# Kernel tuning notes

Measured on AMD Instinct MI355X. Metric: run time of the kernel, lower is better.

The kernel has to match this reference:

```python
import jax, jax.numpy as jnp
import numpy as np

ROWS, COLS, BATCH, NC, DEG = 256, 512, 512, 5, 16
N = (ROWS + COLS) * BATCH            # total nodes
E = ROWS * DEG * BATCH               # total edges
EPS = 1e-07

def _idx_sets():
    blk = np.arange(BATCH)[:, None] * (ROWS + COLS)
    idx_check = (blk + np.arange(ROWS)[None, :]).ravel()          # index_one
    idx_var = (blk + ROWS + np.arange(COLS)[None, :]).ravel()      # index_two
    return jnp.asarray(idx_check, jnp.int32), jnp.asarray(idx_var, jnp.int32)

IDX_CHECK, IDX_VAR = _idx_sets()

def setup_inputs() -> dict:
    key = jax.random.key(0)
    ks = jax.random.split(key, 18)
    rng = np.random.default_rng(0)
    # per-graph block offsets; row0 = check node ids, row1 = variable ids BEFORE the +ROWS shift
    offs = np.repeat(np.arange(BATCH) * (ROWS + COLS), ROWS * DEG)
    src = offs + rng.integers(0, ROWS, size=E)
    dst = offs + rng.integers(0, COLS, size=E)
    edge_index = jnp.asarray(np.stack([src, dst]), jnp.int32)
    x = jax.random.normal(ks[0], (N, 1), jnp.float32)

    def p(k, shape, fan):
        return (jax.random.uniform(k, shape, jnp.float32) * 2.0 - 1.0) / np.sqrt(fan)

    inp = {"x": x, "edge_index": edge_index}
    for li, base in ((1, 1), (2, 9)):
        inp[f"w1_{li}"] = p(ks[base + 0], (10, 2), 2)
        inp[f"b1_{li}"] = p(ks[base + 1], (10,), 2)
        inp[f"w2_{li}"] = p(ks[base + 2], (1, 10), 10)
        inp[f"b2_{li}"] = p(ks[base + 3], (1,), 10)
        inp[f"wih_{li}"] = p(ks[base + 4], (3, 1), 1)
        inp[f"whh_{li}"] = p(ks[base + 5], (3, 1), 1)
        inp[f"bih_{li}"] = p(ks[base + 6], (3,), 1)
        inp[f"bhh_{li}"] = p(ks[base + 7], (3,), 1)
    return inp

def _ggc(h, j_idx, i_idx, agg_idx, upd_idx, w1, b1, w2, b2, wih, whh, bih, bhh):
    # message: mlp(cat[x_j, x_i])
    feat = jnp.concatenate([h[j_idx], h[i_idx]], axis=1)          # [E,2]
    hid = jax.nn.relu(feat @ w1.T + b1)                            # [E,10]
    msg = hid @ w2.T + b2                                          # [E,1]
    m = jax.ops.segment_sum(msg, agg_idx, num_segments=N)          # scatter-add -> [N,1]
    # GRUCell(input=h[idx], hx=m[idx])   (note: original passes old state as INPUT, message as HIDDEN)
    xg = h[upd_idx]
    hx = m[upd_idx]
    gi = xg @ wih.T + bih                                          # [K,3]
    gh = hx @ whh.T + bhh                                          # [K,3]
    r = jax.nn.sigmoid(gi[:, 0:1] + gh[:, 0:1])
    z = jax.nn.sigmoid(gi[:, 1:2] + gh[:, 1:2])
    n = jnp.tanh(gi[:, 2:3] + r * gh[:, 2:3])
    hnew = (1.0 - z) * n + z * hx
    return h.at[upd_idx].set(hnew)

def reference(x, edge_index, w1_1, b1_1, w2_1, b2_1, wih_1, whh_1, bih_1, bhh_1,
              w1_2, b1_2, w2_2, b2_2, wih_2, whh_2, bih_2, bhh_2):
    src = edge_index[0]
    dst = edge_index[1] + ROWS          # shift variable ids into node index space
    h = x
    for _ in range(NC):
        # ggc1: source_to_target -> x_j=h[src], x_i=h[dst], aggregate at dst, update variable nodes
        h = _ggc(h, src, dst, dst, IDX_VAR, w1_1, b1_1, w2_1, b2_1, wih_1, whh_1, bih_1, bhh_1)
        # ggc2: target_to_source -> x_j=h[dst], x_i=h[src], aggregate at src, update check nodes
        h = _ggc(h, dst, src, src, IDX_CHECK, w1_2, b1_2, w2_2, b2_2, wih_2, whh_2, bih_2, bhh_2)
    return jnp.clip(jax.nn.sigmoid(-h), EPS, 1.0 - EPS)
```

## Files before the change

kernel.cpp:

```cpp
#include <hip/hip_runtime.h>

#define ROWS 256
#define COLS 512
#define BATCH 512
#define NC 5
#define DEG 16
#define EPG (ROWS * DEG)
#define NPG (ROWS + COLS)
#define NT 512
#define EPT (EPG / NT)
#define EPSF 1e-7f
#define MV_W (EPG + 3 * COLS)
#define MC_W (EPG + 3 * ROWS)

typedef unsigned short u16;
typedef unsigned int   u32;
typedef float v2f __attribute__((ext_vector_type(2)));

__device__ __forceinline__ float sigmoid_f(float a) {
    return 1.0f / (1.0f + __expf(-a));
}
__device__ __forceinline__ float tanh_f(float a) {
    return fmaf(2.0f, 1.0f / (1.0f + __expf(-2.0f * a)), -1.0f);
}

__global__ __launch_bounds__(NT, 4) void gnni_kernel(
    const float* __restrict__ x,
    const int*   __restrict__ eidx,
    const float* __restrict__ w1_1, const float* __restrict__ b1_1,
    const float* __restrict__ w2_1, const float* __restrict__ b2_1,
    const float* __restrict__ wih_1, const float* __restrict__ whh_1,
    const float* __restrict__ bih_1, const float* __restrict__ bhh_1,
    const float* __restrict__ w1_2, const float* __restrict__ b1_2,
    const float* __restrict__ w2_2, const float* __restrict__ b2_2,
    const float* __restrict__ wih_2, const float* __restrict__ whh_2,
    const float* __restrict__ bih_2, const float* __restrict__ bhh_2,
    float* __restrict__ out)
{
    __shared__ float msgV[MV_W];
    __shared__ float msgC[MC_W];
    __shared__ u32  cntd[COLS];
    __shared__ u32  cnts[ROWS];
    __shared__ u16  beg_v[COLS];
    __shared__ u16  deg_v[COLS];
    __shared__ u16  beg_c[ROWS];
    __shared__ u16  deg_c[ROWS];
    __shared__ float hc[ROWS];
    __shared__ float hv[COLS];
    __shared__ u32  wsum[8];
    __shared__ u32  wsum2[4];

    const int tid  = threadIdx.x;
    const int lane = tid & 63;
    const int wid  = tid >> 6;
    const int b    = blockIdx.x;
    const int base = b * NPG;
    const long ebase = (long)b * EPG;

    const int4 sa = *(const int4*)(eidx + ebase + tid * 8);
    const int4 sb = *(const int4*)(eidx + ebase + tid * 8 + 4);
    const int4 da = *(const int4*)(eidx + (long)BATCH * EPG + ebase + tid * 8);
    const int4 db = *(const int4*)(eidx + (long)BATCH * EPG + ebase + tid * 8 + 4);
    const int sarr[EPT] = {sa.x, sa.y, sa.z, sa.w, sb.x, sb.y, sb.z, sb.w};
    const int darr[EPT] = {da.x, da.y, da.z, da.w, db.x, db.y, db.z, db.w};
    u32 ep[EPT];
    #pragma unroll
    for (int i = 0; i < EPT; ++i)
        ep[i] = (u32)(sarr[i] - base) | ((u32)(darr[i] - base) << 16);

    for (int i = tid; i < MV_W; i += NT) msgV[i] = 0.0f;
    for (int i = tid; i < MC_W; i += NT) msgC[i] = 0.0f;
    cntd[tid] = 0;
    if (tid < ROWS) cnts[tid] = 0;
    __syncthreads();

    #pragma unroll
    for (int i = 0; i < EPT; ++i) {
        atomicAdd(&cntd[ep[i] >> 16], 1u);
        atomicAdd(&cnts[ep[i] & 0xffffu], 1u);
    }
    __syncthreads();

    u32 myd = cntd[tid];
    u32 acd = (myd + 3u) & ~3u;
    u32 scv = acd;
    #pragma unroll
    for (int st = 1; st < 64; st <<= 1) {
        u32 t = __shfl_up(scv, st);
        if (lane >= st) scv += t;
    }
    if (lane == 63) wsum[wid] = scv;
    u32 mys = 0, acs = 0, scc = 0;
    if (tid < ROWS) {
        mys = cnts[tid];
        acs = (mys + 3u) & ~3u;
        scc = acs;
        #pragma unroll
        for (int st = 1; st < 64; st <<= 1) {
            u32 t = __shfl_up(scc, st);
            if (lane >= st) scc += t;
        }
        if (lane == 63) wsum2[wid] = scc;
    }
    __syncthreads();
    if (tid < 8) {
        u32 v = wsum[tid];
        #pragma unroll
        for (int st = 1; st < 8; st <<= 1) {
            u32 t = __shfl_up(v, st);
            if (tid >= st) v += t;
        }
        wsum[tid] = v;
    } else if (tid < 12) {
        u32 v = wsum2[tid - 8];
        #pragma unroll
        for (int st = 1; st < 4; st <<= 1) {
            u32 t = __shfl_up(v, st);
            if (tid - 8 >= st) v += t;
        }
        wsum2[tid - 8] = v;
    }
    __syncthreads();
    {
        u32 inc  = scv + (wid ? wsum[wid - 1] : 0u);
        u32 begv = inc - acd;
        beg_v[tid] = (u16)begv;
        deg_v[tid] = (u16)myd;
        cntd[tid]  = begv;
    }
    if (tid < ROWS) {
        u32 inc  = scc + (wid ? wsum2[wid - 1] : 0u);
        u32 begc = inc - acs;
        beg_c[tid] = (u16)begc;
        deg_c[tid] = (u16)mys;
        cnts[tid]  = begc;
        hc[tid] = x[base + tid];
    }
    float hvreg = x[base + ROWS + tid];
    hv[tid] = hvreg;
    __syncthreads();

    u32 aS[EPT], aD[EPT], p1B[EPT], p2B[EPT];
    #pragma unroll
    for (int i = 0; i < EPT; ++i) {
        const u32 p = ep[i];
        const u32 s = p & 0xffffu;
        const u32 d = p >> 16;
        aS[i]  = s << 2;
        aD[i]  = d << 2;
        p1B[i] = atomicAdd(&cntd[d], 1u) << 2;
        p2B[i] = atomicAdd(&cnts[s], 1u) << 2;
    }

    v2f A1[5], C1[5], B1[5], W1[5], A2[5], C2[5], B2[5], W2[5];
    #pragma unroll
    for (int j = 0; j < 5; ++j) {
        A1[j] = (v2f){w1_1[4*j],     w1_1[4*j + 2]};
        C1[j] = (v2f){w1_1[4*j + 1], w1_1[4*j + 3]};
        B1[j] = (v2f){b1_1[2*j],     b1_1[2*j + 1]};
        W1[j] = (v2f){w2_1[2*j],     w2_1[2*j + 1]};
        A2[j] = (v2f){w1_2[4*j],     w1_2[4*j + 2]};
        C2[j] = (v2f){w1_2[4*j + 1], w1_2[4*j + 3]};
        B2[j] = (v2f){b1_2[2*j],     b1_2[2*j + 1]};
        W2[j] = (v2f){w2_2[2*j],     w2_2[2*j + 1]};
    }
    const float b2_1s = b2_1[0], b2_2s = b2_2[0];
    const v2f zero2 = (v2f){0.0f, 0.0f};
    const char* const hcB   = (const char*)hc;
    const char* const hvB   = (const char*)hv;
    char*       const msgVB = (char*)msgV;
    char*       const msgCB = (char*)msgC;

    for (int it = 0; it < NC; ++it) {
        float hcs[EPT];
        #pragma unroll
        for (int i = 0; i < EPT; ++i) hcs[i] = *(const float*)(hcB + aS[i]);

        #pragma unroll
        for (int i = 0; i < EPT; ++i) {
            const float xj = hcs[i];
            const float xi = *(const float*)(hvB + aD[i]);
            const v2f xj2 = (v2f){xj, xj}, xi2 = (v2f){xi, xi};
            v2f acc = (v2f){b2_1s, 0.0f};
            #pragma unroll
            for (int j = 0; j < 5; ++j) {
                v2f t = __builtin_elementwise_fma(C1[j], xi2, B1[j]);
                t = __builtin_elementwise_fma(A1[j], xj2, t);
                t = __builtin_elementwise_max(t, zero2);
                acc = __builtin_elementwise_fma(W1[j], t, acc);
            }
            *(float*)(msgVB + p1B[i]) = acc.x + acc.y;
        }
        __syncthreads();

        {
            const int beg = beg_v[tid];
            const int deg = deg_v[tid];
            const float4* mp = (const float4*)&msgV[beg];
            float4 a4 = {0.0f, 0.0f, 0.0f, 0.0f};
            #pragma unroll
            for (int k = 0; k < 5; ++k) {
                if (4 * k < deg) {
                    const float4 q = mp[k];
                    a4.x += q.x; a4.y += q.y; a4.z += q.z; a4.w += q.w;
                }
            }
            float hx = (a4.x + a4.y) + (a4.z + a4.w);
            for (int e = beg + 20; e < beg + deg; ++e) hx += msgV[e];
            const float xg = hvreg;
            float gi0 = fmaf(wih_1[0], xg, bih_1[0]);
            float gi1 = fmaf(wih_1[1], xg, bih_1[1]);
            float gi2 = fmaf(wih_1[2], xg, bih_1[2]);
            float gh0 = fmaf(whh_1[0], hx, bhh_1[0]);
            float gh1 = fmaf(whh_1[1], hx, bhh_1[1]);
            float gh2 = fmaf(whh_1[2], hx, bhh_1[2]);
            float r = sigmoid_f(gi0 + gh0);
            float z = sigmoid_f(gi1 + gh1);
            float n = tanh_f(fmaf(r, gh2, gi2));
            hvreg = fmaf(1.0f - z, n, z * hx);
            hv[tid] = hvreg;
        }
        __syncthreads();

        #pragma unroll
        for (int i = 0; i < EPT; ++i) {
            const float xi = hcs[i];
            const float xj = *(const float*)(hvB + aD[i]);
            const v2f xj2 = (v2f){xj, xj}, xi2 = (v2f){xi, xi};
            v2f acc = (v2f){b2_2s, 0.0f};
            #pragma unroll
            for (int j = 0; j < 5; ++j) {
                v2f t = __builtin_elementwise_fma(C2[j], xi2, B2[j]);
                t = __builtin_elementwise_fma(A2[j], xj2, t);
                t = __builtin_elementwise_max(t, zero2);
                acc = __builtin_elementwise_fma(W2[j], t, acc);
            }
            *(float*)(msgCB + p2B[i]) = acc.x + acc.y;
        }
        __syncthreads();

        {
            const int c    = tid >> 1;
            const int half = tid & 1;
            const int beg = beg_c[c];
            const int deg = deg_c[c];
            const float4* mp = (const float4*)&msgC[beg];
            float4 a4 = {0.0f, 0.0f, 0.0f, 0.0f};
            #pragma unroll
            for (int k = 0; k < 4; ++k) {
                const int ch = half + 2 * k;
                if (4 * ch < deg) {
                    const float4 q = mp[ch];
                    a4.x += q.x; a4.y += q.y; a4.z += q.z; a4.w += q.w;
                }
            }
            float part = (a4.x + a4.y) + (a4.z + a4.w);
            for (int e = beg + 32 + half; e < beg + deg; e += 2) part += msgC[e];
            part += __shfl_xor(part, 1);
            if (half == 0) {
                const float hx = part;
                const float xg = hc[c];
                float gi0 = fmaf(wih_2[0], xg, bih_2[0]);
                float gi1 = fmaf(wih_2[1], xg, bih_2[1]);
                float gi2 = fmaf(wih_2[2], xg, bih_2[2]);
                float gh0 = fmaf(whh_2[0], hx, bhh_2[0]);
                float gh1 = fmaf(whh_2[1], hx, bhh_2[1]);
                float gh2 = fmaf(whh_2[2], hx, bhh_2[2]);
                float r = sigmoid_f(gi0 + gh0);
                float z = sigmoid_f(gi1 + gh1);
                float n = tanh_f(fmaf(r, gh2, gi2));
                hc[c] = fmaf(1.0f - z, n, z * hx);
            }
        }
        __syncthreads();
    }

    {
        float sgm = 1.0f / (1.0f + __expf(hvreg));
        out[base + ROWS + tid] = fminf(fmaxf(sgm, EPSF), 1.0f - EPSF);
    }
    if (tid < ROWS) {
        float sgm = 1.0f / (1.0f + __expf(hc[tid]));
        out[base + tid] = fminf(fmaxf(sgm, EPSF), 1.0f - EPSF);
    }
}

extern "C" void kernel_launch(void* const* d_in, const int* in_sizes, int n_in,
                              void* d_out, int out_size, void* d_ws, size_t ws_size,
                              hipStream_t stream) {
    const float* x    = (const float*)d_in[0];
    const int*   eidx = (const int*)d_in[1];
    gnni_kernel<<<BATCH, NT, 0, stream>>>(
        x, eidx,
        (const float*)d_in[2],  (const float*)d_in[3],
        (const float*)d_in[4],  (const float*)d_in[5],
        (const float*)d_in[6],  (const float*)d_in[7],
        (const float*)d_in[8],  (const float*)d_in[9],
        (const float*)d_in[10], (const float*)d_in[11],
        (const float*)d_in[12], (const float*)d_in[13],
        (const float*)d_in[14], (const float*)d_in[15],
        (const float*)d_in[16], (const float*)d_in[17],
        (float*)d_out);
}
```

Measured before the change: 38.44 us.

## Double threads per block and split edge and reduction work across more lanes

Raises the block size from 512 to 1024 threads, so each thread handles 4 edges instead of 8. The variable-node reduction is now split across 2 lanes and the check-node reduction across 4 lanes, combined with shuffles. The count-scan phases are remapped onto separate wave ranges, and the final output write is unified. The aim is to shorten the serial per-iteration work within each graph block by using more waves per CU. The cost is more lanes idling in the GRU update phases and higher register and occupancy pressure at 1024 threads with the unchanged launch bounds.

```diff
diff --git a/kernel.cpp b/kernel.cpp
--- a/kernel.cpp
+++ b/kernel.cpp
@@ -7,7 +7,7 @@
 #define DEG 16
 #define EPG (ROWS * DEG)
 #define NPG (ROWS + COLS)
-#define NT 512
+#define NT 1024
 #define EPT (EPG / NT)
 #define EPSF 1e-7f
 #define MV_W (EPG + 3 * COLS)
@@ -57,42 +57,45 @@
     const int base = b * NPG;
     const long ebase = (long)b * EPG;
 
-    const int4 sa = *(const int4*)(eidx + ebase + tid * 8);
-    const int4 sb = *(const int4*)(eidx + ebase + tid * 8 + 4);
-    const int4 da = *(const int4*)(eidx + (long)BATCH * EPG + ebase + tid * 8);
-    const int4 db = *(const int4*)(eidx + (long)BATCH * EPG + ebase + tid * 8 + 4);
-    const int sarr[EPT] = {sa.x, sa.y, sa.z, sa.w, sb.x, sb.y, sb.z, sb.w};
-    const int darr[EPT] = {da.x, da.y, da.z, da.w, db.x, db.y, db.z, db.w};
-    u32 ep[EPT];
+    const int4 sa = *(const int4*)(eidx + ebase + tid * 4);
+    const int4 da = *(const int4*)(eidx + (long)BATCH * EPG + ebase + tid * 4);
+    const int sarr[EPT] = {sa.x, sa.y, sa.z, sa.w};
+    const int darr[EPT] = {da.x, da.y, da.z, da.w};
+    u32 sloc[EPT], dloc[EPT];
     #pragma unroll
-    for (int i = 0; i < EPT; ++i)
-        ep[i] = (u32)(sarr[i] - base) | ((u32)(darr[i] - base) << 16);
+    for (int i = 0; i < EPT; ++i) {
+        sloc[i] = (u32)(sarr[i] - base);
+        dloc[i] = (u32)(darr[i] - base);
+    }
 
     for (int i = tid; i < MV_W; i += NT) msgV[i] = 0.0f;
     for (int i = tid; i < MC_W; i += NT) msgC[i] = 0.0f;
-    cntd[tid] = 0;
-    if (tid < ROWS) cnts[tid] = 0;
+    if (tid < COLS) cntd[tid] = 0;
+    else if (tid - COLS < ROWS) cnts[tid - COLS] = 0;
     __syncthreads();
 
     #pragma unroll
     for (int i = 0; i < EPT; ++i) {
-        atomicAdd(&cntd[ep[i] >> 16], 1u);
-        atomicAdd(&cnts[ep[i] & 0xffffu], 1u);
-    }
-    __syncthreads();
-
-    u32 myd = cntd[tid];
-    u32 acd = (myd + 3u) & ~3u;
-    u32 scv = acd;
-    #pragma unroll
-    for (int st = 1; st < 64; st <<= 1) {
-        u32 t = __shfl_up(scv, st);
-        if (lane >= st) scv += t;
-    }
-    if (lane == 63) wsum[wid] = scv;
+        atomicAdd(&cntd[dloc[i]], 1u);
+        atomicAdd(&cnts[sloc[i]], 1u);
+    }
+    __syncthreads();
+
+    u32 myd = 0, acd = 0, scv = 0;
+    if (tid < COLS) {
+        myd = cntd[tid];
+        acd = (myd + 3u) & ~3u;
+        scv = acd;
+        #pragma unroll
+        for (int st = 1; st < 64; st <<= 1) {
+            u32 t = __shfl_up(scv, st);
+            if (lane >= st) scv += t;
+        }
+        if (lane == 63) wsum[wid] = scv;
+    }
     u32 mys = 0, acs = 0, scc = 0;
-    if (tid < ROWS) {
-        mys = cnts[tid];
+    if (tid >= 512 && tid < 512 + ROWS) {
+        mys = cnts[tid - 512];
         acs = (mys + 3u) & ~3u;
         scc = acs;
         #pragma unroll
@@ -100,7 +103,7 @@
             u32 t = __shfl_up(scc, st);
             if (lane >= st) scc += t;
         }
-        if (lane == 63) wsum2[wid] = scc;
+        if (lane == 63) wsum2[wid - 8] = scc;
     }
     __syncthreads();
     if (tid < 8) {
@@ -121,35 +124,32 @@
         wsum2[tid - 8] = v;
     }
     __syncthreads();
-    {
+    if (tid < COLS) {
         u32 inc  = scv + (wid ? wsum[wid - 1] : 0u);
         u32 begv = inc - acd;
         beg_v[tid] = (u16)begv;
         deg_v[tid] = (u16)myd;
         cntd[tid]  = begv;
     }
-    if (tid < ROWS) {
-        u32 inc  = scc + (wid ? wsum2[wid - 1] : 0u);
+    if (tid >= 512 && tid < 512 + ROWS) {
+        int w2 = wid - 8;
+        u32 inc  = scc + (w2 ? wsum2[w2 - 1] : 0u);
         u32 begc = inc - acs;
-        beg_c[tid] = (u16)begc;
-        deg_c[tid] = (u16)mys;
-        cnts[tid]  = begc;
-        hc[tid] = x[base + tid];
-    }
-    float hvreg = x[base + ROWS + tid];
-    hv[tid] = hvreg;
+        beg_c[tid - 512] = (u16)begc;
+        deg_c[tid - 512] = (u16)mys;
+        cnts[tid - 512]  = begc;
+    }
+    if (tid < ROWS) hc[tid] = x[base + tid];
+    else if (tid < NPG) hv[tid - ROWS] = x[base + tid];
     __syncthreads();
 
     u32 aS[EPT], aD[EPT], p1B[EPT], p2B[EPT];
     #pragma unroll
     for (int i = 0; i < EPT; ++i) {
-        const u32 p = ep[i];
-        const u32 s = p & 0xffffu;
-        const u32 d = p >> 16;
-        aS[i]  = s << 2;
-        aD[i]  = d << 2;
-        p1B[i] = atomicAdd(&cntd[d], 1u) << 2;
-        p2B[i] = atomicAdd(&cnts[s], 1u) << 2;
+        aS[i]  = sloc[i] << 2;
+        aD[i]  = dloc[i] << 2;
+        p1B[i] = atomicAdd(&cntd[dloc[i]], 1u) << 2;
+        p2B[i] = atomicAdd(&cnts[sloc[i]], 1u) << 2;
     }
 
     v2f A1[5], C1[5], B1[5], W1[5], A2[5], C2[5], B2[5], W2[5];
@@ -194,31 +194,37 @@
         __syncthreads();
 
         {
-            const int beg = beg_v[tid];
-            const int deg = deg_v[tid];
+            const int v    = tid >> 1;
+            const int half = tid & 1;
+            const int beg = beg_v[v];
+            const int deg = deg_v[v];
             const float4* mp = (const float4*)&msgV[beg];
             float4 a4 = {0.0f, 0.0f, 0.0f, 0.0f};
             #pragma unroll
-            for (int k = 0; k < 5; ++k) {
-                if (4 * k < deg) {
-                    const float4 q = mp[k];
+            for (int k = 0; k < 3; ++k) {
+                const int ch = half + 2 * k;
+                if (4 * ch < deg) {
+                    const float4 q = mp[ch];
                     a4.x += q.x; a4.y += q.y; a4.z += q.z; a4.w += q.w;
                 }
             }
-            float hx = (a4.x + a4.y) + (a4.z + a4.w);
-            for (int e = beg + 20; e < beg + deg; ++e) hx += msgV[e];
-            const float xg = hvreg;
-            float gi0 = fmaf(wih_1[0], xg, bih_1[0]);
-            float gi1 = fmaf(wih_1[1], xg, bih_1[1]);
-            float gi2 = fmaf(wih_1[2], xg, bih_1[2]);
-            float gh0 = fmaf(whh_1[0], hx, bhh_1[0]);
-            float gh1 = fmaf(whh_1[1], hx, bhh_1[1]);
-            float gh2 = fmaf(whh_1[2], hx, bhh_1[2]);
-            float r = sigmoid_f(gi0 + gh0);
-            float z = sigmoid_f(gi1 + gh1);
-            float n = tanh_f(fmaf(r, gh2, gi2));
-            hvreg = fmaf(1.0f - z, n, z * hx);
-            hv[tid] = hvreg;
+            float part = (a4.x + a4.y) + (a4.z + a4.w);
+            for (int e = beg + 24 + half; e < beg + deg; e += 2) part += msgV[e];
+            part += __shfl_xor(part, 1);
+            if (half == 0) {
+                const float hx = part;
+                const float xg = hv[v];
+                float gi0 = fmaf(wih_1[0], xg, bih_1[0]);
+                float gi1 = fmaf(wih_1[1], xg, bih_1[1]);
+                float gi2 = fmaf(wih_1[2], xg, bih_1[2]);
+                float gh0 = fmaf(whh_1[0], hx, bhh_1[0]);
+                float gh1 = fmaf(whh_1[1], hx, bhh_1[1]);
+                float gh2 = fmaf(whh_1[2], hx, bhh_1[2]);
+                float r = sigmoid_f(gi0 + gh0);
+                float z = sigmoid_f(gi1 + gh1);
+                float n = tanh_f(fmaf(r, gh2, gi2));
+                hv[v] = fmaf(1.0f - z, n, z * hx);
+            }
         }
         __syncthreads();
 
@@ -240,24 +246,25 @@
         __syncthreads();
 
         {
-            const int c    = tid >> 1;
-            const int half = tid & 1;
+            const int c  = tid >> 2;
+            const int q4 = tid & 3;
             const int beg = beg_c[c];
             const int deg = deg_c[c];
             const float4* mp = (const float4*)&msgC[beg];
             float4 a4 = {0.0f, 0.0f, 0.0f, 0.0f};
             #pragma unroll
-            for (int k = 0; k < 4; ++k) {
-                const int ch = half + 2 * k;
+            for (int k = 0; k < 2; ++k) {
+                const int ch = q4 + 4 * k;
                 if (4 * ch < deg) {
                     const float4 q = mp[ch];
                     a4.x += q.x; a4.y += q.y; a4.z += q.z; a4.w += q.w;
                 }
             }
             float part = (a4.x + a4.y) + (a4.z + a4.w);
-            for (int e = beg + 32 + half; e < beg + deg; e += 2) part += msgC[e];
+            for (int e = beg + 32 + q4; e < beg + deg; e += 4) part += msgC[e];
             part += __shfl_xor(part, 1);
-            if (half == 0) {
+            part += __shfl_xor(part, 2);
+            if (q4 == 0) {
                 const float hx = part;
                 const float xg = hc[c];
                 float gi0 = fmaf(wih_2[0], xg, bih_2[0]);
@@ -275,12 +282,9 @@
         __syncthreads();
     }
 
-    {
-        float sgm = 1.0f / (1.0f + __expf(hvreg));
-        out[base + ROWS + tid] = fminf(fmaxf(sgm, EPSF), 1.0f - EPSF);
-    }
-    if (tid < ROWS) {
-        float sgm = 1.0f / (1.0f + __expf(hc[tid]));
+    if (tid < NPG) {
+        float h = (tid < ROWS) ? hc[tid] : hv[tid - ROWS];
+        float sgm = 1.0f / (1.0f + __expf(h));
         out[base + tid] = fminf(fmaxf(sgm, EPSF), 1.0f - EPSF);
     }
 }
```

Result: slower. 47.42 us (+23.4%).

## Process two graphs per block to amortize barriers and raise per-thread ILP

Applied to the files above, without the earlier changes.

Each block now handles two graphs (GPB=2): shared arrays are doubled, edges, atomics, scans and the message/GRU phases are interleaved across both graphs, and the grid is halved. The variable-node values per edge are also cached in registers (hvs) and reloaded only after the variable update, instead of being re-read from LDS in every phase. This aims to amortize the per-iteration syncthreads and increase independent work per wave. The cost is double the LDS per block and more registers, with launch bounds lowered to 2 blocks per CU, which reduces occupancy and leaves only 256 blocks for the whole GPU.

```diff
diff --git a/kernel.cpp b/kernel.cpp
--- a/kernel.cpp
+++ b/kernel.cpp
@@ -9,6 +9,7 @@
 #define NPG (ROWS + COLS)
 #define NT 512
 #define EPT (EPG / NT)
+#define GPB 2
 #define EPSF 1e-7f
 #define MV_W (EPG + 3 * COLS)
 #define MC_W (EPG + 3 * ROWS)
@@ -24,7 +25,7 @@
     return fmaf(2.0f, 1.0f / (1.0f + __expf(-2.0f * a)), -1.0f);
 }
 
-__global__ __launch_bounds__(NT, 4) void gnni_kernel(
+__global__ __launch_bounds__(NT, 2) void gnni_kernel(
     const float* __restrict__ x,
     const int*   __restrict__ eidx,
     const float* __restrict__ w1_1, const float* __restrict__ b1_1,
@@ -37,120 +38,148 @@
     const float* __restrict__ bih_2, const float* __restrict__ bhh_2,
     float* __restrict__ out)
 {
-    __shared__ float msgV[MV_W];
-    __shared__ float msgC[MC_W];
-    __shared__ u32  cntd[COLS];
-    __shared__ u32  cnts[ROWS];
-    __shared__ u16  beg_v[COLS];
-    __shared__ u16  deg_v[COLS];
-    __shared__ u16  beg_c[ROWS];
-    __shared__ u16  deg_c[ROWS];
-    __shared__ float hc[ROWS];
-    __shared__ float hv[COLS];
-    __shared__ u32  wsum[8];
-    __shared__ u32  wsum2[4];
+    __shared__ float msgV[GPB][MV_W];
+    __shared__ float msgC[GPB][MC_W];
+    __shared__ u32  cntd[GPB][COLS];
+    __shared__ u32  cnts[GPB][ROWS];
+    __shared__ u16  beg_v[GPB][COLS];
+    __shared__ u16  deg_v[GPB][COLS];
+    __shared__ u16  beg_c[GPB][ROWS];
+    __shared__ u16  deg_c[GPB][ROWS];
+    __shared__ float hc[GPB][ROWS];
+    __shared__ float hv[GPB][COLS];
+    __shared__ u32  wsum[GPB][8];
+    __shared__ u32  wsum2[GPB][4];
 
     const int tid  = threadIdx.x;
     const int lane = tid & 63;
     const int wid  = tid >> 6;
     const int b    = blockIdx.x;
-    const int base = b * NPG;
-    const long ebase = (long)b * EPG;
-
-    const int4 sa = *(const int4*)(eidx + ebase + tid * 8);
-    const int4 sb = *(const int4*)(eidx + ebase + tid * 8 + 4);
-    const int4 da = *(const int4*)(eidx + (long)BATCH * EPG + ebase + tid * 8);
-    const int4 db = *(const int4*)(eidx + (long)BATCH * EPG + ebase + tid * 8 + 4);
-    const int sarr[EPT] = {sa.x, sa.y, sa.z, sa.w, sb.x, sb.y, sb.z, sb.w};
-    const int darr[EPT] = {da.x, da.y, da.z, da.w, db.x, db.y, db.z, db.w};
-    u32 ep[EPT];
-    #pragma unroll
-    for (int i = 0; i < EPT; ++i)
-        ep[i] = (u32)(sarr[i] - base) | ((u32)(darr[i] - base) << 16);
-
-    for (int i = tid; i < MV_W; i += NT) msgV[i] = 0.0f;
-    for (int i = tid; i < MC_W; i += NT) msgC[i] = 0.0f;
-    cntd[tid] = 0;
-    if (tid < ROWS) cnts[tid] = 0;
-    __syncthreads();
-
-    #pragma unroll
-    for (int i = 0; i < EPT; ++i) {
-        atomicAdd(&cntd[ep[i] >> 16], 1u);
-        atomicAdd(&cnts[ep[i] & 0xffffu], 1u);
-    }
-    __syncthreads();
-
-    u32 myd = cntd[tid];
-    u32 acd = (myd + 3u) & ~3u;
-    u32 scv = acd;
+    int  baseg[GPB];
+    long ebaseg[GPB];
+    #pragma unroll
+    for (int g = 0; g < GPB; ++g) {
+        baseg[g]  = (GPB * b + g) * NPG;
+        ebaseg[g] = (long)(GPB * b + g) * EPG;
+    }
+
+    u32 aS[GPB][EPT], aD[GPB][EPT];
+    #pragma unroll
+    for (int g = 0; g < GPB; ++g) {
+        const int4 sa = *(const int4*)(eidx + ebaseg[g] + tid * 8);
+        const int4 sb = *(const int4*)(eidx + ebaseg[g] + tid * 8 + 4);
+        const int4 da = *(const int4*)(eidx + (long)BATCH * EPG + ebaseg[g] + tid * 8);
+        const int4 db = *(const int4*)(eidx + (long)BATCH * EPG + ebaseg[g] + tid * 8 + 4);
+        const int sarr[EPT] = {sa.x, sa.y, sa.z, sa.w, sb.x, sb.y, sb.z, sb.w};
+        const int darr[EPT] = {da.x, da.y, da.z, da.w, db.x, db.y, db.z, db.w};
+        #pragma unroll
+        for (int i = 0; i < EPT; ++i) {
+            aS[g][i] = (u32)(sarr[i] - baseg[g]) << 2;
+            aD[g][i] = (u32)(darr[i] - baseg[g]) << 2;
+        }
+    }
+
+    for (int i = tid; i < MV_W; i += NT) { msgV[0][i] = 0.0f; msgV[1][i] = 0.0f; }
+    for (int i = tid; i < MC_W; i += NT) { msgC[0][i] = 0.0f; msgC[1][i] = 0.0f; }
+    cntd[0][tid] = 0; cntd[1][tid] = 0;
+    if (tid < ROWS) { cnts[0][tid] = 0; cnts[1][tid] = 0; }
+    __syncthreads();
+
+    #pragma unroll
+    for (int g = 0; g < GPB; ++g)
+        #pragma unroll
+        for (int i = 0; i < EPT; ++i) {
+            atomicAdd(&cntd[g][aD[g][i] >> 2], 1u);
+            atomicAdd(&cnts[g][aS[g][i] >> 2], 1u);
+        }
+    __syncthreads();
+
+    u32 myd[GPB], acd[GPB], scv[GPB];
+    #pragma unroll
+    for (int g = 0; g < GPB; ++g) {
+        myd[g] = cntd[g][tid];
+        acd[g] = (myd[g] + 3u) & ~3u;
+        scv[g] = acd[g];
+    }
     #pragma unroll
     for (int st = 1; st < 64; st <<= 1) {
-        u32 t = __shfl_up(scv, st);
-        if (lane >= st) scv += t;
-    }
-    if (lane == 63) wsum[wid] = scv;
-    u32 mys = 0, acs = 0, scc = 0;
+        u32 t0 = __shfl_up(scv[0], st);
+        u32 t1 = __shfl_up(scv[1], st);
+        if (lane >= st) { scv[0] += t0; scv[1] += t1; }
+    }
+    if (lane == 63) { wsum[0][wid] = scv[0]; wsum[1][wid] = scv[1]; }
+    u32 mys[GPB] = {0, 0}, acs[GPB] = {0, 0}, scc[GPB] = {0, 0};
     if (tid < ROWS) {
-        mys = cnts[tid];
-        acs = (mys + 3u) & ~3u;
-        scc = acs;
+        #pragma unroll
+        for (int g = 0; g < GPB; ++g) {
+            mys[g] = cnts[g][tid];
+            acs[g] = (mys[g] + 3u) & ~3u;
+            scc[g] = acs[g];
+        }
         #pragma unroll
         for (int st = 1; st < 64; st <<= 1) {
-            u32 t = __shfl_up(scc, st);
-            if (lane >= st) scc += t;
-        }
-        if (lane == 63) wsum2[wid] = scc;
+            u32 t0 = __shfl_up(scc[0], st);
+            u32 t1 = __shfl_up(scc[1], st);
+            if (lane >= st) { scc[0] += t0; scc[1] += t1; }
+        }
+        if (lane == 63) { wsum2[0][wid] = scc[0]; wsum2[1][wid] = scc[1]; }
     }
     __syncthreads();
     if (tid < 8) {
-        u32 v = wsum[tid];
+        u32 v0 = wsum[0][tid], v1 = wsum[1][tid];
         #pragma unroll
         for (int st = 1; st < 8; st <<= 1) {
-            u32 t = __shfl_up(v, st);
-            if (tid >= st) v += t;
-        }
-        wsum[tid] = v;
+            u32 t0 = __shfl_up(v0, st);
+            u32 t1 = __shfl_up(v1, st);
+            if (tid >= st) { v0 += t0; v1 += t1; }
+        }
+        wsum[0][tid] = v0; wsum[1][tid] = v1;
     } else if (tid < 12) {
-        u32 v = wsum2[tid - 8];
+        u32 v0 = wsum2[0][tid - 8], v1 = wsum2[1][tid - 8];
         #pragma unroll
         for (int st = 1; st < 4; st <<= 1) {
-            u32 t = __shfl_up(v, st);
-            if (tid - 8 >= st) v += t;
-        }
-        wsum2[tid - 8] = v;
-    }
-    __syncthreads();
-    {
-        u32 inc  = scv + (wid ? wsum[wid - 1] : 0u);
-        u32 begv = inc - acd;
-        beg_v[tid] = (u16)begv;
-        deg_v[tid] = (u16)myd;
-        cntd[tid]  = begv;
+            u32 t0 = __shfl_up(v0, st);
+            u32 t1 = __shfl_up(v1, st);
+            if (tid - 8 >= st) { v0 += t0; v1 += t1; }
+        }
+        wsum2[0][tid - 8] = v0; wsum2[1][tid - 8] = v1;
+    }
+    __syncthreads();
+    #pragma unroll
+    for (int g = 0; g < GPB; ++g) {
+        u32 inc  = scv[g] + (wid ? wsum[g][wid - 1] : 0u);
+        u32 begv = inc - acd[g];
+        beg_v[g][tid] = (u16)begv;
+        deg_v[g][tid] = (u16)myd[g];
+        cntd[g][tid]  = begv;
     }
     if (tid < ROWS) {
-        u32 inc  = scc + (wid ? wsum2[wid - 1] : 0u);
-        u32 begc = inc - acs;
-        beg_c[tid] = (u16)begc;
-        deg_c[tid] = (u16)mys;
-        cnts[tid]  = begc;
-        hc[tid] = x[base + tid];
-    }
-    float hvreg = x[base + ROWS + tid];
-    hv[tid] = hvreg;
-    __syncthreads();
-
-    u32 aS[EPT], aD[EPT], p1B[EPT], p2B[EPT];
-    #pragma unroll
-    for (int i = 0; i < EPT; ++i) {
-        const u32 p = ep[i];
-        const u32 s = p & 0xffffu;
-        const u32 d = p >> 16;
-        aS[i]  = s << 2;
-        aD[i]  = d << 2;
-        p1B[i] = atomicAdd(&cntd[d], 1u) << 2;
-        p2B[i] = atomicAdd(&cnts[s], 1u) << 2;
-    }
+        #pragma unroll
+        for (int g = 0; g < GPB; ++g) {
+            u32 inc  = scc[g] + (wid ? wsum2[g][wid - 1] : 0u);
+            u32 begc = inc - acs[g];
+            beg_c[g][tid] = (u16)begc;
+            deg_c[g][tid] = (u16)mys[g];
+            cnts[g][tid]  = begc;
+            hc[g][tid] = x[baseg[g] + tid];
+        }
+    }
+    float hvreg[GPB];
+    #pragma unroll
+    for (int g = 0; g < GPB; ++g) {
+        hvreg[g] = x[baseg[g] + ROWS + tid];
+        hv[g][tid] = hvreg[g];
+    }
+    __syncthreads();
+
+    u32 p1B[GPB][EPT], p2B[GPB][EPT];
+    #pragma unroll
+    for (int g = 0; g < GPB; ++g)
+        #pragma unroll
+        for (int i = 0; i < EPT; ++i) {
+            p1B[g][i] = atomicAdd(&cntd[g][aD[g][i] >> 2], 1u) << 2;
+            p2B[g][i] = atomicAdd(&cnts[g][aS[g][i] >> 2], 1u) << 2;
+        }
 
     v2f A1[5], C1[5], B1[5], W1[5], A2[5], C2[5], B2[5], W2[5];
     #pragma unroll
@@ -166,37 +195,46 @@
     }
     const float b2_1s = b2_1[0], b2_2s = b2_2[0];
     const v2f zero2 = (v2f){0.0f, 0.0f};
-    const char* const hcB   = (const char*)hc;
-    const char* const hvB   = (const char*)hv;
-    char*       const msgVB = (char*)msgV;
-    char*       const msgCB = (char*)msgC;
+
+    float hvs[GPB][EPT];
+    #pragma unroll
+    for (int g = 0; g < GPB; ++g)
+        #pragma unroll
+        for (int i = 0; i < EPT; ++i)
+            hvs[g][i] = *(const float*)((const char*)&hv[g][0] + aD[g][i]);
 
     for (int it = 0; it < NC; ++it) {
-        float hcs[EPT];
-        #pragma unroll
-        for (int i = 0; i < EPT; ++i) hcs[i] = *(const float*)(hcB + aS[i]);
-
-        #pragma unroll
-        for (int i = 0; i < EPT; ++i) {
-            const float xj = hcs[i];
-            const float xi = *(const float*)(hvB + aD[i]);
-            const v2f xj2 = (v2f){xj, xj}, xi2 = (v2f){xi, xi};
-            v2f acc = (v2f){b2_1s, 0.0f};
-            #pragma unroll
-            for (int j = 0; j < 5; ++j) {
-                v2f t = __builtin_elementwise_fma(C1[j], xi2, B1[j]);
-                t = __builtin_elementwise_fma(A1[j], xj2, t);
-                t = __builtin_elementwise_max(t, zero2);
-                acc = __builtin_elementwise_fma(W1[j], t, acc);
+        float hcs[GPB][EPT];
+        #pragma unroll
+        for (int g = 0; g < GPB; ++g)
+            #pragma unroll
+            for (int i = 0; i < EPT; ++i)
+                hcs[g][i] = *(const float*)((const char*)&hc[g][0] + aS[g][i]);
+
+        #pragma unroll
+        for (int g = 0; g < GPB; ++g)
+            #pragma unroll
+            for (int i = 0; i < EPT; ++i) {
+                const float xj = hcs[g][i];
+                const float xi = hvs[g][i];
+                const v2f xj2 = (v2f){xj, xj}, xi2 = (v2f){xi, xi};
+                v2f acc = (v2f){b2_1s, 0.0f};
+                #pragma unroll
+                for (int j = 0; j < 5; ++j) {
+                    v2f t = __builtin_elementwise_fma(C1[j], xi2, B1[j]);
+                    t = __builtin_elementwise_fma(A1[j], xj2, t);
+                    t = __builtin_elementwise_max(t, zero2);
+                    acc = __builtin_elementwise_fma(W1[j], t, acc);
+                }
+                *(float*)((char*)&msgV[g][0] + p1B[g][i]) = acc.x + acc.y;
             }
-            *(float*)(msgVB + p1B[i]) = acc.x + acc.y;
-        }
         __syncthreads();
 
-        {
-            const int beg = beg_v[tid];
-            const int deg = deg_v[tid];
-            const float4* mp = (const float4*)&msgV[beg];
+        #pragma unroll
+        for (int g = 0; g < GPB; ++g) {
+            const int beg = beg_v[g][tid];
+            const int deg = deg_v[g][tid];
+            const float4* mp = (const float4*)&msgV[g][beg];
             float4 a4 = {0.0f, 0.0f, 0.0f, 0.0f};
             #pragma unroll
             for (int k = 0; k < 5; ++k) {
@@ -206,8 +244,8 @@
                 }
             }
             float hx = (a4.x + a4.y) + (a4.z + a4.w);
-            for (int e = beg + 20; e < beg + deg; ++e) hx += msgV[e];
-            const float xg = hvreg;
+            for (int e = beg + 20; e < beg + deg; ++e) hx += msgV[g][e];
+            const float xg = hvreg[g];
             float gi0 = fmaf(wih_1[0], xg, bih_1[0]);
             float gi1 = fmaf(wih_1[1], xg, bih_1[1]);
             float gi2 = fmaf(wih_1[2], xg, bih_1[2]);
@@ -217,71 +255,82 @@
             float r = sigmoid_f(gi0 + gh0);
             float z = sigmoid_f(gi1 + gh1);
             float n = tanh_f(fmaf(r, gh2, gi2));
-            hvreg = fmaf(1.0f - z, n, z * hx);
-            hv[tid] = hvreg;
+            hvreg[g] = fmaf(1.0f - z, n, z * hx);
+            hv[g][tid] = hvreg[g];
         }
         __syncthreads();
 
         #pragma unroll
-        for (int i = 0; i < EPT; ++i) {
-            const float xi = hcs[i];
-            const float xj = *(const float*)(hvB + aD[i]);
-            const v2f xj2 = (v2f){xj, xj}, xi2 = (v2f){xi, xi};
-            v2f acc = (v2f){b2_2s, 0.0f};
-            #pragma unroll
-            for (int j = 0; j < 5; ++j) {
-                v2f t = __builtin_elementwise_fma(C2[j], xi2, B2[j]);
-                t = __builtin_elementwise_fma(A2[j], xj2, t);
-                t = __builtin_elementwise_max(t, zero2);
-                acc = __builtin_elementwise_fma(W2[j], t, acc);
+        for (int g = 0; g < GPB; ++g)
+            #pragma unroll
+            for (int i = 0; i < EPT; ++i)
+                hvs[g][i] = *(const float*)((const char*)&hv[g][0] + aD[g][i]);
+        #pragma unroll
+        for (int g = 0; g < GPB; ++g)
+            #pragma unroll
+            for (int i = 0; i < EPT; ++i) {
+                const float xi = hcs[g][i];
+                const float xj = hvs[g][i];
+                const v2f xj2 = (v2f){xj, xj}, xi2 = (v2f){xi, xi};
+                v2f acc = (v2f){b2_2s, 0.0f};
+                #pragma unroll
+                for (int j = 0; j < 5; ++j) {
+                    v2f t = __builtin_elementwise_fma(C2[j], xi2, B2[j]);
+                    t = __builtin_elementwise_fma(A2[j], xj2, t);
+                    t = __builtin_elementwise_max(t, zero2);
+                    acc = __builtin_elementwise_fma(W2[j], t, acc);
+                }
+                *(float*)((char*)&msgC[g][0] + p2B[g][i]) = acc.x + acc.y;
             }
-            *(float*)(msgCB + p2B[i]) = acc.x + acc.y;
-        }
         __syncthreads();
 
         {
             const int c    = tid >> 1;
             const int half = tid & 1;
-            const int beg = beg_c[c];
-            const int deg = deg_c[c];
-            const float4* mp = (const float4*)&msgC[beg];
-            float4 a4 = {0.0f, 0.0f, 0.0f, 0.0f};
-            #pragma unroll
-            for (int k = 0; k < 4; ++k) {
-                const int ch = half + 2 * k;
-                if (4 * ch < deg) {
-                    const float4 q = mp[ch];
-                    a4.x += q.x; a4.y += q.y; a4.z += q.z; a4.w += q.w;
+            #pragma unroll
+            for (int g = 0; g < GPB; ++g) {
+                const int beg = beg_c[g][c];
+                const int deg = deg_c[g][c];
+                const float4* mp = (const float4*)&msgC[g][beg];
+                float4 a4 = {0.0f, 0.0f, 0.0f, 0.0f};
+                #pragma unroll
+                for (int k = 0; k < 4; ++k) {
+                    const int ch = half + 2 * k;
+                    if (4 * ch < deg) {
+                        const float4 q = mp[ch];
+                        a4.x += q.x; a4.y += q.y; a4.z += q.z; a4.w += q.w;
+                    }
+                }
+                float part = (a4.x + a4.y) + (a4.z + a4.w);
+                for (int e = beg + 32 + half; e < beg + deg; e += 2) part += msgC[g][e];
+                part += __shfl_xor(part, 1);
+                if (half == 0) {
+                    const float hx = part;
+                    const float xg = hc[g][c];
+                    float gi0 = fmaf(wih_2[0], xg, bih_2[0]);
+                    float gi1 = fmaf(wih_2[1], xg, bih_2[1]);
+                    float gi2 = fmaf(wih_2[2], xg, bih_2[2]);
+                    float gh0 = fmaf(whh_2[0], hx, bhh_2[0]);
+                    float gh1 = fmaf(whh_2[1], hx, bhh_2[1]);
+                    float gh2 = fmaf(whh_2[2], hx, bhh_2[2]);
+                    float r = sigmoid_f(gi0 + gh0);
+                    float z = sigmoid_f(gi1 + gh1);
+                    float n = tanh_f(fmaf(r, gh2, gi2));
+                    hc[g][c] = fmaf(1.0f - z, n, z * hx);
                 }
             }
-            float part = (a4.x + a4.y) + (a4.z + a4.w);
-            for (int e = beg + 32 + half; e < beg + deg; e += 2) part += msgC[e];
-            part += __shfl_xor(part, 1);
-            if (half == 0) {
-                const float hx = part;
-                const float xg = hc[c];
-                float gi0 = fmaf(wih_2[0], xg, bih_2[0]);
-                float gi1 = fmaf(wih_2[1], xg, bih_2[1]);
-                float gi2 = fmaf(wih_2[2], xg, bih_2[2]);
-                float gh0 = fmaf(whh_2[0], hx, bhh_2[0]);
-                float gh1 = fmaf(whh_2[1], hx, bhh_2[1]);
-                float gh2 = fmaf(whh_2[2], hx, bhh_2[2]);
-                float r = sigmoid_f(gi0 + gh0);
-                float z = sigmoid_f(gi1 + gh1);
-                float n = tanh_f(fmaf(r, gh2, gi2));
-                hc[c] = fmaf(1.0f - z, n, z * hx);
-            }
         }
         __syncthreads();
     }
 
-    {
-        float sgm = 1.0f / (1.0f + __expf(hvreg));
-        out[base + ROWS + tid] = fminf(fmaxf(sgm, EPSF), 1.0f - EPSF);
-    }
-    if (tid < ROWS) {
-        float sgm = 1.0f / (1.0f + __expf(hc[tid]));
-        out[base + tid] = fminf(fmaxf(sgm, EPSF), 1.0f - EPSF);
+    #pragma unroll
+    for (int g = 0; g < GPB; ++g) {
+        float sgm = 1.0f / (1.0f + __expf(hvreg[g]));
+        out[baseg[g] + ROWS + tid] = fminf(fmaxf(sgm, EPSF), 1.0f - EPSF);
+        if (tid < ROWS) {
+            float s2 = 1.0f / (1.0f + __expf(hc[g][tid]));
+            out[baseg[g] + tid] = fminf(fmaxf(s2, EPSF), 1.0f - EPSF);
+        }
     }
 }
 
@@ -290,7 +339,7 @@
                               hipStream_t stream) {
     const float* x    = (const float*)d_in[0];
     const int*   eidx = (const int*)d_in[1];
-    gnni_kernel<<<BATCH, NT, 0, stream>>>(
+    gnni_kernel<<<BATCH / GPB, NT, 0, stream>>>(
         x, eidx,
         (const float*)d_in[2],  (const float*)d_in[3],
         (const float*)d_in[4],  (const float*)d_in[5],
```

Result: slower. 42.64 us (+10.9%).
